# Optimization experiments

Measured on AMD Instinct MI355X. Metric: run time of the kernel, lower is better.

## Reference

```python
import jax, jax.numpy as jnp
import numpy as np

N = 4_000_000      # total rows across all strata
D = 64             # covariate dimension (nn.Linear input_size)
N_SEG = 100_000    # number of strata (groups)


def setup_inputs() -> dict:
    key = jax.random.key(0)
    k1, k2, k3, k4 = jax.random.split(key, 4)
    X = jax.random.normal(k1, (N, D), dtype=jnp.float32)
    # sorted segment ids encode the ragged strata lengths (rows are packed per group)
    seg_ids = jnp.sort(jax.random.randint(k2, (N,), 0, N_SEG)).astype(jnp.int32)
    w = jax.random.normal(k3, (D,), dtype=jnp.float32) * 0.1
    b = jax.random.normal(k4, (1,), dtype=jnp.float32)
    return {"X": X, "seg_ids": seg_ids, "w": w, "b": b}


def reference(X, seg_ids, w, b):
    # linear projection to a single logit per row: y_hat = X @ w + b
    logits = X @ w + b[0]                                   # [N]
    # segment softmax == padded (-300) row softmax with padding underflowing to 0
    m = jax.ops.segment_max(logits, seg_ids, num_segments=N_SEG)   # [N_SEG]
    m = jnp.where(jnp.isfinite(m), m, jnp.float32(0.0))            # guard empty segments
    z = jnp.exp(logits - m[seg_ids])                               # [N]
    denom = jax.ops.segment_sum(z, seg_ids, num_segments=N_SEG)    # [N_SEG]
    return z / denom[seg_ids]                                      # [N] per-group softmax probs
```

## Files before the change

### kernel.cpp

```cpp
#include <hip/hip_runtime.h>
#include <math.h>

#define NROWS 4000000
#define DCOV  64
#define NSEG  100000

__global__ void logits_kernel(const float* __restrict__ X,
                              const float* __restrict__ w,
                              const float* __restrict__ b,
                              float* __restrict__ logits,
                              int ngroups ) {
    const int lane        = threadIdx.x & 63;
    const int waveInBlock = threadIdx.x >> 6;
    const int wavesPerBlk = blockDim.x >> 6;
    const int sub         = lane & 15;
    const int rowInGroup  = lane >> 4;

    long long gwave  = (long long)blockIdx.x * wavesPerBlk + waveInBlock;
    long long nwaves = (long long)gridDim.x * wavesPerBlk;

    const float4 w4 = reinterpret_cast<const float4*>(w)[sub];
    const float bias = b[0];

    for (long long g = gwave; g < ngroups; g += nwaves) {
        const float4* xp = reinterpret_cast<const float4*>(X) + g * 64;
        float4 x = xp[lane];
        float p = x.x * w4.x + x.y * w4.y + x.z * w4.z + x.w * w4.w;
        p += __shfl_xor(p, 1);
        p += __shfl_xor(p, 2);
        p += __shfl_xor(p, 4);
        p += __shfl_xor(p, 8);
        if (sub == 0) {
            logits[g * 4 + rowInGroup] = p + bias;
        }
    }
}

__global__ void init_bounds_kernel(int* __restrict__ seg_start,
                                   int* __restrict__ seg_end, int nseg) {
    int i = blockIdx.x * blockDim.x + threadIdx.x;
    if (i < nseg) { seg_start[i] = 0; seg_end[i] = 0; }
}

__global__ void find_bounds_kernel(const int* __restrict__ seg,
                                   int* __restrict__ seg_start,
                                   int* __restrict__ seg_end, int n) {
    int i = blockIdx.x * blockDim.x + threadIdx.x;
    if (i >= n) return;
    int s = seg[i];
    if (i == 0     || seg[i - 1] != s) seg_start[s] = i;
    if (i == n - 1 || seg[i + 1] != s) seg_end[s]   = i + 1;
}

__global__ void seg_softmax_kernel(const float* __restrict__ logits,
                                   const int* __restrict__ seg_start,
                                   const int* __restrict__ seg_end,
                                   float* __restrict__ out, int nseg) {
    const int lane = threadIdx.x & 63;
    const int wave = threadIdx.x >> 6;
    const int s = blockIdx.x * (blockDim.x >> 6) + wave;
    if (s >= nseg) return;

    const int start = seg_start[s];
    const int end   = seg_end[s];
    const int len   = end - start;

    if (len <= 64) {
        const bool act = lane < len;
        float x = act ? logits[start + lane] : -INFINITY;
        float mx = x;
        #pragma unroll
        for (int m = 1; m < 64; m <<= 1) mx = fmaxf(mx, __shfl_xor(mx, m));
        float e = act ? __expf(x - mx) : 0.0f;
        float sum = e;
        #pragma unroll
        for (int m = 1; m < 64; m <<= 1) sum += __shfl_xor(sum, m);
        if (act) out[start + lane] = e / sum;
    } else {
        float mx = -INFINITY;
        for (int i = start + lane; i < end; i += 64) mx = fmaxf(mx, logits[i]);
        #pragma unroll
        for (int m = 1; m < 64; m <<= 1) mx = fmaxf(mx, __shfl_xor(mx, m));
        float sum = 0.0f;
        for (int i = start + lane; i < end; i += 64) sum += __expf(logits[i] - mx);
        #pragma unroll
        for (int m = 1; m < 64; m <<= 1) sum += __shfl_xor(sum, m);
        const float inv = 1.0f / sum;
        for (int i = start + lane; i < end; i += 64)
            out[i] = __expf(logits[i] - mx) * inv;
    }
}

extern "C" void kernel_launch(void* const* d_in, const int* in_sizes, int n_in,
                              void* d_out, int out_size, void* d_ws, size_t ws_size,
                              hipStream_t stream) {
    const float* X    = (const float*)d_in[0];
    const int*   seg  = (const int*)d_in[1];
    const float* w    = (const float*)d_in[2];
    const float* b    = (const float*)d_in[3];
    float*       out  = (float*)d_out;

    float* logits    = (float*)d_ws;
    int*   seg_start = (int*)((char*)d_ws + (size_t)NROWS * sizeof(float));
    int*   seg_end   = seg_start + NSEG;

    const int ngroups = NROWS / 4;
    logits_kernel<<<2048, 256, 0, stream>>>(X, w, b, logits, ngroups);

    init_bounds_kernel<<<(NSEG + 255) / 256, 256, 0, stream>>>(seg_start, seg_end, NSEG);
    find_bounds_kernel<<<NROWS / 256, 256, 0, stream>>>(seg, seg_start, seg_end, NROWS);

    const int wavesPerBlock = 4;
    const int nblocks = (NSEG + wavesPerBlock - 1) / wavesPerBlock;
    seg_softmax_kernel<<<nblocks, wavesPerBlock * 64, 0, stream>>>(
        logits, seg_start, seg_end, out, NSEG);
}
```

Baseline: 224.4 us.

## Fuse logits and segment-bounds passes into one launch with CSR offsets

Merges the logits projection and the segment-boundary computation into one kernel, with separate block ranges for each job, so the two independent passes can run concurrently and two launches plus the init kernel go away. Boundaries become a single offsets array of NSEG+1 entries, filled so empty segments are covered without a separate zeroing pass. The logits loop now handles two 4-row groups per iteration using nontemporal loads, for more memory-level parallelism and less cache pollution from X. In exchange, the boundary-writing loops can be long if there are gaps in the segment ids.

```diff
diff --git a/kernel.cpp b/kernel.cpp
--- a/kernel.cpp
+++ b/kernel.cpp
@@ -5,64 +5,76 @@
 #define DCOV  64
 #define NSEG  100000
 
-__global__ void logits_kernel(const float* __restrict__ X,
-                              const float* __restrict__ w,
-                              const float* __restrict__ b,
-                              float* __restrict__ logits,
-                              int ngroups ) {
-    const int lane        = threadIdx.x & 63;
-    const int waveInBlock = threadIdx.x >> 6;
-    const int wavesPerBlk = blockDim.x >> 6;
-    const int sub         = lane & 15;
-    const int rowInGroup  = lane >> 4;
+#define LOGITS_BLOCKS 2048
+#define BOUNDS_BLOCKS 512
 
-    long long gwave  = (long long)blockIdx.x * wavesPerBlk + waveInBlock;
-    long long nwaves = (long long)gridDim.x * wavesPerBlk;
+typedef float f32x4 __attribute__((ext_vector_type(4)));
 
-    const float4 w4 = reinterpret_cast<const float4*>(w)[sub];
-    const float bias = b[0];
+__global__ void fused_logits_bounds_kernel(const float* __restrict__ X,
+                                           const float* __restrict__ w,
+                                           const float* __restrict__ b,
+                                           const int* __restrict__ seg,
+                                           float* __restrict__ logits,
+                                           int* __restrict__ st) {
+    if (blockIdx.x < LOGITS_BLOCKS) {
+        const int lane        = threadIdx.x & 63;
+        const int waveInBlock = threadIdx.x >> 6;
+        const int sub         = lane & 15;
+        const int rowInGroup  = lane >> 4;
 
-    for (long long g = gwave; g < ngroups; g += nwaves) {
-        const float4* xp = reinterpret_cast<const float4*>(X) + g * 64;
-        float4 x = xp[lane];
-        float p = x.x * w4.x + x.y * w4.y + x.z * w4.z + x.w * w4.w;
-        p += __shfl_xor(p, 1);
-        p += __shfl_xor(p, 2);
-        p += __shfl_xor(p, 4);
-        p += __shfl_xor(p, 8);
-        if (sub == 0) {
-            logits[g * 4 + rowInGroup] = p + bias;
+        const long long nwaves = (long long)LOGITS_BLOCKS * 4;
+        const long long gwave  = (long long)blockIdx.x * 4 + waveInBlock;
+        const long long npairs = NROWS / 8;
+
+        const float4 w4 = reinterpret_cast<const float4*>(w)[sub];
+        const float bias = b[0];
+
+        const f32x4* Xv = reinterpret_cast<const f32x4*>(X);
+
+        for (long long p = gwave; p < npairs; p += nwaves) {
+            const f32x4* xp = Xv + p * 128;
+            f32x4 x0 = __builtin_nontemporal_load(xp + lane);
+            f32x4 x1 = __builtin_nontemporal_load(xp + 64 + lane);
+            float p0 = x0.x * w4.x + x0.y * w4.y + x0.z * w4.z + x0.w * w4.w;
+            float p1 = x1.x * w4.x + x1.y * w4.y + x1.z * w4.z + x1.w * w4.w;
+            p0 += __shfl_xor(p0, 1);  p1 += __shfl_xor(p1, 1);
+            p0 += __shfl_xor(p0, 2);  p1 += __shfl_xor(p1, 2);
+            p0 += __shfl_xor(p0, 4);  p1 += __shfl_xor(p1, 4);
+            p0 += __shfl_xor(p0, 8);  p1 += __shfl_xor(p1, 8);
+            if (sub == 0) {
+                logits[p * 8 + rowInGroup]     = p0 + bias;
+                logits[p * 8 + 4 + rowInGroup] = p1 + bias;
+            }
+        }
+    } else {
+        const long long tid    = (long long)(blockIdx.x - LOGITS_BLOCKS) * blockDim.x
+                               + threadIdx.x;
+        const long long stride = (long long)BOUNDS_BLOCKS * blockDim.x;
+        for (long long i = tid; i < NROWS; i += stride) {
+            int s = seg[i];
+            if (i == 0) {
+                for (int t = 0; t <= s; ++t) st[t] = 0;
+            } else {
+                int prev = seg[i - 1];
+                for (int t = prev + 1; t <= s; ++t) st[t] = (int)i;
+            }
+            if (i == NROWS - 1) {
+                for (int t = s + 1; t <= NSEG; ++t) st[t] = NROWS;
+            }
         }
     }
 }
 
-__global__ void init_bounds_kernel(int* __restrict__ seg_start,
-                                   int* __restrict__ seg_end, int nseg) {
-    int i = blockIdx.x * blockDim.x + threadIdx.x;
-    if (i < nseg) { seg_start[i] = 0; seg_end[i] = 0; }
-}
-
-__global__ void find_bounds_kernel(const int* __restrict__ seg,
-                                   int* __restrict__ seg_start,
-                                   int* __restrict__ seg_end, int n) {
-    int i = blockIdx.x * blockDim.x + threadIdx.x;
-    if (i >= n) return;
-    int s = seg[i];
-    if (i == 0     || seg[i - 1] != s) seg_start[s] = i;
-    if (i == n - 1 || seg[i + 1] != s) seg_end[s]   = i + 1;
-}
-
 __global__ void seg_softmax_kernel(const float* __restrict__ logits,
-                                   const int* __restrict__ seg_start,
-                                   const int* __restrict__ seg_end,
+                                   const int* __restrict__ st,
                                    float* __restrict__ out, int nseg) {
     const int lane = threadIdx.x & 63;
     const int wave = threadIdx.x >> 6;
     const int s = blockIdx.x * (blockDim.x >> 6) + wave;
     if (s >= nseg) return;
 
-    const int start = seg_start[s];
-    const int end   = seg_end[s];
+    const int start = st[s];
+    const int end   = st[s + 1];
     const int len   = end - start;
 
     if (len <= 64) {
@@ -94,24 +106,20 @@
 extern "C" void kernel_launch(void* const* d_in, const int* in_sizes, int n_in,
                               void* d_out, int out_size, void* d_ws, size_t ws_size,
                               hipStream_t stream) {
-    const float* X    = (const float*)d_in[0];
-    const int*   seg  = (const int*)d_in[1];
-    const float* w    = (const float*)d_in[2];
-    const float* b    = (const float*)d_in[3];
-    float*       out  = (float*)d_out;
+    const float* X   = (const float*)d_in[0];
+    const int*   seg = (const int*)d_in[1];
+    const float* w   = (const float*)d_in[2];
+    const float* b   = (const float*)d_in[3];
+    float*       out = (float*)d_out;
 
-    float* logits    = (float*)d_ws;
-    int*   seg_start = (int*)((char*)d_ws + (size_t)NROWS * sizeof(float));
-    int*   seg_end   = seg_start + NSEG;
+    float* logits = (float*)d_ws;
+    int*   st     = (int*)((char*)d_ws + (size_t)NROWS * sizeof(float));
 
-    const int ngroups = NROWS / 4;
-    logits_kernel<<<2048, 256, 0, stream>>>(X, w, b, logits, ngroups);
-
-    init_bounds_kernel<<<(NSEG + 255) / 256, 256, 0, stream>>>(seg_start, seg_end, NSEG);
-    find_bounds_kernel<<<NROWS / 256, 256, 0, stream>>>(seg, seg_start, seg_end, NROWS);
+    fused_logits_bounds_kernel<<<LOGITS_BLOCKS + BOUNDS_BLOCKS, 256, 0, stream>>>(
+        X, w, b, seg, logits, st);
 
     const int wavesPerBlock = 4;
     const int nblocks = (NSEG + wavesPerBlock - 1) / wavesPerBlock;
     seg_softmax_kernel<<<nblocks, wavesPerBlock * 64, 0, stream>>>(
-        logits, seg_start, seg_end, out, NSEG);
+        logits, st, out, NSEG);
 }
```

After: 216.9 us. 3.3% less time.
